# Performance work log

Measured on AMD Instinct MI355X. Metric: run time of the kernel, lower is better.

The kernel has to match this reference:

```python
import jax, jax.numpy as jnp
import numpy as np

DIM = 1024
HEAD_NUM = 8
D_HEAD = DIM // HEAD_NUM
B, S = 4, 2048


def setup_inputs() -> dict:
    key = jax.random.key(0)
    ks = jax.random.split(key, 7)
    scale = 0.02
    return {
        "Q": jax.random.normal(ks[0], (B, S, DIM), dtype=jnp.float32),
        "K": jax.random.normal(ks[1], (B, S, DIM), dtype=jnp.float32),
        "V": jax.random.normal(ks[2], (B, S, DIM), dtype=jnp.float32),
        "W_Q": jax.random.normal(ks[3], (DIM, DIM), dtype=jnp.float32) * scale,
        "W_K": jax.random.normal(ks[4], (DIM, DIM), dtype=jnp.float32) * scale,
        "W_V": jax.random.normal(ks[5], (DIM, DIM), dtype=jnp.float32) * scale,
        "W_O": jax.random.normal(ks[6], (DIM, DIM), dtype=jnp.float32) * scale,
    }


def reference(Q, K, V, W_Q, W_K, W_V, W_O):
    # torch nn.Linear(bias=False): y = x @ W.T
    b, s, d = Q.shape
    h, dh = HEAD_NUM, d // HEAD_NUM

    def proj_split(x, W):
        # split_head: tensor_split along feature dim into h contiguous chunks,
        # stack at dim 1 -> [b, h, s, dh]; equivalent to reshape+transpose.
        y = jnp.einsum('bsd,ed->bse', x, W)
        return y.reshape(b, s, h, dh).transpose(0, 2, 1, 3)

    q = proj_split(Q, W_Q)  # [b,h,s,dh]
    k = proj_split(K, W_K)
    v = proj_split(V, W_V)

    scores = jnp.einsum('bhqd,bhkd->bhqk', q, k) / jnp.sqrt(jnp.float32(dh))
    # FAITHFUL to original: nn.Softmax(dim=1) normalizes over the HEAD axis.
    attn = jax.nn.softmax(scores, axis=1)
    # dropout is identity in eval mode
    ctx = jnp.einsum('bhqk,bhkd->bhqd', attn, v)  # [b,h,s,dh]
    # concat_head: heads concatenated back along feature dim in order
    ctx = ctx.transpose(0, 2, 1, 3).reshape(b, s, d)
    return jnp.einsum('bsd,ed->bse', ctx, W_O)
```

## Files before the change

### kernel.cpp

```cpp
#include <hip/hip_runtime.h>
#include <math.h>
#include <stdint.h>


typedef __attribute__((ext_vector_type(8))) __bf16 bf16x8;
typedef __attribute__((ext_vector_type(4))) __bf16 bf16x4;
typedef __attribute__((ext_vector_type(4))) float  f32x4;

__device__ __forceinline__ f32x4 mfma16(bf16x8 a, bf16x8 b, f32x4 c) {
    return __builtin_amdgcn_mfma_f32_16x16x32_bf16(a, b, c, 0, 0, 0);
}

__device__ __forceinline__ void cp16(void* lds, const void* g) {
    __builtin_amdgcn_global_load_lds(
        (__attribute__((address_space(1))) void*)(void*)(const_cast<void*>(g)),
        (__attribute__((address_space(3))) void*)lds,
        16, 0, 0);
}

__global__ void cast_f32_to_bf16(const float* __restrict__ src,
                                 __bf16* __restrict__ dst, int n4) {
    int i = blockIdx.x * blockDim.x + threadIdx.x;
    const int stride = gridDim.x * blockDim.x;
    for (; i < n4; i += stride) {
        float4 f = ((const float4*)src)[i];
        bf16x4 o;
        o[0] = (__bf16)f.x; o[1] = (__bf16)f.y; o[2] = (__bf16)f.z; o[3] = (__bf16)f.w;
        ((bf16x4*)dst)[i] = o;
    }
}

__global__ void cast4_f32_to_bf16(const float* __restrict__ s0, __bf16* __restrict__ d0,
                                  const float* __restrict__ s1, __bf16* __restrict__ d1,
                                  const float* __restrict__ s2, __bf16* __restrict__ d2,
                                  const float* __restrict__ s3, __bf16* __restrict__ d3,
                                  int n4) {
    const float* s = (blockIdx.y == 0) ? s0 : (blockIdx.y == 1) ? s1
                    : (blockIdx.y == 2) ? s2 : s3;
    __bf16* d = (blockIdx.y == 0) ? d0 : (blockIdx.y == 1) ? d1
               : (blockIdx.y == 2) ? d2 : d3;
    int i = blockIdx.x * blockDim.x + threadIdx.x;
    const int stride = gridDim.x * blockDim.x;
    for (; i < n4; i += stride) {
        float4 f = ((const float4*)s)[i];
        bf16x4 o;
        o[0] = (__bf16)f.x; o[1] = (__bf16)f.y; o[2] = (__bf16)f.z; o[3] = (__bf16)f.w;
        ((bf16x4*)d)[i] = o;
    }
}

template<int MODE>
__global__ __launch_bounds__(256, 2) void gemm_bt(const __bf16* __restrict__ A,
                                                  const __bf16* __restrict__ Bt,
                                                  void* __restrict__ out,
                                                  float scale)
{
    __shared__ __bf16 As[128 * 32];
    __shared__ __bf16 Bs[128 * 32];
    const int tid  = threadIdx.x;
    const int lane = tid & 63;
    const int u = lane >> 4, v = lane & 15;
    const int w = tid >> 6;
    const int wm = (w >> 1) * 64, wn = (w & 1) * 64;
    const long tM = (long)blockIdx.y * 128;
    const int  tN = blockIdx.x * 128;

    f32x4 acc[4][4];
#pragma unroll
    for (int i = 0; i < 4; ++i)
#pragma unroll
        for (int j = 0; j < 4; ++j) acc[i][j] = (f32x4){0.f, 0.f, 0.f, 0.f};

    const int c0 = tid, c1 = tid + 256;
    const int ar0 = c0 >> 2, ak0 = (c0 & 3) * 8;
    const int ar1 = c1 >> 2, ak1 = (c1 & 3) * 8;

    const __bf16* Ab = A  + tM * 1024;
    const __bf16* Bb = Bt + (long)tN * 1024;

    for (int k0 = 0; k0 < 1024; k0 += 32) {
        __syncthreads();
        cp16(&As[ar0 * 32 + ak0], Ab + (long)ar0 * 1024 + k0 + ak0);
        cp16(&As[ar1 * 32 + ak1], Ab + (long)ar1 * 1024 + k0 + ak1);
        cp16(&Bs[ar0 * 32 + ak0], Bb + (long)ar0 * 1024 + k0 + ak0);
        cp16(&Bs[ar1 * 32 + ak1], Bb + (long)ar1 * 1024 + k0 + ak1);
        __syncthreads();

        bf16x8 af[4], bfr[4];
#pragma unroll
        for (int i = 0; i < 4; ++i)
            af[i] = *(const bf16x8*)&As[(wm + i * 16 + v) * 32 + u * 8];
#pragma unroll
        for (int j = 0; j < 4; ++j)
            bfr[j] = *(const bf16x8*)&Bs[(wn + j * 16 + v) * 32 + u * 8];
#pragma unroll
        for (int i = 0; i < 4; ++i)
#pragma unroll
            for (int j = 0; j < 4; ++j)
                acc[i][j] = mfma16(af[i], bfr[j], acc[i][j]);
    }

#pragma unroll
    for (int i = 0; i < 4; ++i) {
#pragma unroll
        for (int j = 0; j < 4; ++j) {
            const long row0 = tM + wm + i * 16 + u * 4;
            const int  col  = tN + wn + j * 16 + v;
            if (MODE == 0) {
                __bf16* o = (__bf16*)out;
#pragma unroll
                for (int r = 0; r < 4; ++r)
                    o[(row0 + r) * 1024 + col] = (__bf16)(acc[i][j][r] * scale);
            } else if (MODE == 1) {
                float* o = (float*)out;
#pragma unroll
                for (int r = 0; r < 4; ++r)
                    o[(row0 + r) * 1024 + col] = acc[i][j][r];
            } else {
                __bf16* o = (__bf16*)out;
                const int bidx = (int)(row0 >> 11);
                const int s    = (int)(row0 & 2047);
                const int h = col >> 7, dh = col & 127;
                bf16x4 pk;
#pragma unroll
                for (int r = 0; r < 4; ++r) pk[r] = (__bf16)acc[i][j][r];
                *(bf16x4*)&o[((long)(bidx * 8 + h) * 128 + dh) * 2048 + s] = pk;
            }
        }
    }
}

__global__ __launch_bounds__(256, 4) void qk_head_softmax(
    const __bf16* __restrict__ kp, const __bf16* __restrict__ qp,
    __bf16* __restrict__ P, int b_base, int q_base)
{
    __shared__ __bf16 As[64 * 32];
    __shared__ __bf16 Bs[128 * 32];
    __shared__ __bf16 tb[128 * 68];
    const int tid  = threadIdx.x;
    const int lane = tid & 63;
    const int u = lane >> 4, v = lane & 15;
    const int w = tid >> 6;
    const int wm = (w >> 1) * 32, wn = (w & 1) * 64;
    const int bloc = blockIdx.z;
    const int b    = b_base + bloc;
    const int k0   = blockIdx.x * 64;
    const int q0l  = blockIdx.y * 128;
    const int q0g  = q_base + q0l;
    const long Cq  = (long)gridDim.y * 128;

    const int ar0 = tid >> 2, ak0 = (tid & 3) * 8;
    const int ar1 = ar0 + 64, ak1 = ak0;

    const __bf16* Ka = kp + ((long)b * 2048 + k0) * 1024;
    const __bf16* Qa = qp + ((long)b * 2048 + q0g) * 1024;

    f32x4 den[2][4];
#pragma unroll
    for (int i = 0; i < 2; ++i)
#pragma unroll
        for (int j = 0; j < 4; ++j) den[i][j] = (f32x4){0.f, 0.f, 0.f, 0.f};

#pragma unroll 1
    for (int h = 0; h < 8; ++h) {
        f32x4 acc[2][4];
#pragma unroll
        for (int i = 0; i < 2; ++i)
#pragma unroll
            for (int j = 0; j < 4; ++j) acc[i][j] = (f32x4){0.f, 0.f, 0.f, 0.f};

#pragma unroll
        for (int kb = 0; kb < 4; ++kb) {
            const int co = h * 128 + kb * 32;
            __syncthreads();
            cp16(&As[ar0 * 32 + ak0], Ka + (long)ar0 * 1024 + co + ak0);
            cp16(&Bs[ar0 * 32 + ak0], Qa + (long)ar0 * 1024 + co + ak0);
            cp16(&Bs[ar1 * 32 + ak1], Qa + (long)ar1 * 1024 + co + ak1);
            __syncthreads();

            bf16x8 af[2], bfr[4];
#pragma unroll
            for (int i = 0; i < 2; ++i)
                af[i] = *(const bf16x8*)&As[(wm + i * 16 + v) * 32 + u * 8];
#pragma unroll
            for (int j = 0; j < 4; ++j)
                bfr[j] = *(const bf16x8*)&Bs[(wn + j * 16 + v) * 32 + u * 8];
#pragma unroll
            for (int i = 0; i < 2; ++i)
#pragma unroll
                for (int j = 0; j < 4; ++j)
                    acc[i][j] = mfma16(af[i], bfr[j], acc[i][j]);
        }
#pragma unroll
        for (int i = 0; i < 2; ++i)
#pragma unroll
            for (int j = 0; j < 4; ++j)
#pragma unroll
                for (int r = 0; r < 4; ++r)
                    den[i][j][r] += __expf(acc[i][j][r]);
    }

#pragma unroll
    for (int i = 0; i < 2; ++i)
#pragma unroll
        for (int j = 0; j < 4; ++j)
#pragma unroll
            for (int r = 0; r < 4; ++r) den[i][j][r] = 1.0f / den[i][j][r];

#pragma unroll 1
    for (int h = 0; h < 8; ++h) {
        f32x4 acc[2][4];
#pragma unroll
        for (int i = 0; i < 2; ++i)
#pragma unroll
            for (int j = 0; j < 4; ++j) acc[i][j] = (f32x4){0.f, 0.f, 0.f, 0.f};

#pragma unroll
        for (int kb = 0; kb < 4; ++kb) {
            const int co = h * 128 + kb * 32;
            __syncthreads();
            cp16(&As[ar0 * 32 + ak0], Ka + (long)ar0 * 1024 + co + ak0);
            cp16(&Bs[ar0 * 32 + ak0], Qa + (long)ar0 * 1024 + co + ak0);
            cp16(&Bs[ar1 * 32 + ak1], Qa + (long)ar1 * 1024 + co + ak1);
            __syncthreads();

            bf16x8 af[2], bfr[4];
#pragma unroll
            for (int i = 0; i < 2; ++i)
                af[i] = *(const bf16x8*)&As[(wm + i * 16 + v) * 32 + u * 8];
#pragma unroll
            for (int j = 0; j < 4; ++j)
                bfr[j] = *(const bf16x8*)&Bs[(wn + j * 16 + v) * 32 + u * 8];
#pragma unroll
            for (int i = 0; i < 2; ++i)
#pragma unroll
                for (int j = 0; j < 4; ++j)
                    acc[i][j] = mfma16(af[i], bfr[j], acc[i][j]);
        }
        __syncthreads();
#pragma unroll
        for (int i = 0; i < 2; ++i)
#pragma unroll
            for (int j = 0; j < 4; ++j) {
                const int kc = wm + i * 16 + u * 4;
                const int qr = wn + j * 16 + v;
                bf16x4 o;
#pragma unroll
                for (int r = 0; r < 4; ++r) {
                    float e = (float)(__bf16)__expf(acc[i][j][r]);
                    o[r] = (__bf16)(e * den[i][j][r]);
                }
                *(bf16x4*)&tb[qr * 68 + kc] = o;
            }
        __syncthreads();
        __bf16* Ph = P + ((long)(bloc * 8 + h) * Cq + q0l) * 2048 + k0;
#pragma unroll
        for (int p = 0; p < 4; ++p) {
            const int qq = p * 32 + (tid >> 3);
            const int kk = (tid & 7) * 8;
            *(bf16x8*)&Ph[(long)qq * 2048 + kk] = *(const bf16x8*)&tb[qq * 68 + kk];
        }
    }
}

__global__ __launch_bounds__(256, 2) void pv_gemm(
    const __bf16* __restrict__ vt, const __bf16* __restrict__ P,
    __bf16* __restrict__ ctx, int b_base, int q_base)
{
    __shared__ __bf16 As[128 * 32];
    __shared__ __bf16 Bs[128 * 32];
    const int tid  = threadIdx.x;
    const int lane = tid & 63;
    const int u = lane >> 4, v = lane & 15;
    const int w = tid >> 6;
    const int wm = (w >> 1) * 64, wn = (w & 1) * 64;
    const int bhl  = blockIdx.y;
    const int bloc = bhl >> 3, h = bhl & 7;
    const int b    = b_base + bloc;
    const int q0l  = blockIdx.x * 128;
    const int q0g  = q_base + q0l;
    const long Cq  = (long)gridDim.x * 128;

    const int c0 = tid, c1 = tid + 256;
    const int ar0 = c0 >> 2, ak0 = (c0 & 3) * 8;
    const int ar1 = c1 >> 2, ak1 = (c1 & 3) * 8;

    const __bf16* Ab = vt + (long)(b * 8 + h) * 128 * 2048;
    const __bf16* Bb = P  + ((long)(bloc * 8 + h) * Cq + q0l) * 2048;

    f32x4 acc[4][4];
#pragma unroll
    for (int i = 0; i < 4; ++i)
#pragma unroll
        for (int j = 0; j < 4; ++j) acc[i][j] = (f32x4){0.f, 0.f, 0.f, 0.f};

    for (int k0 = 0; k0 < 2048; k0 += 32) {
        __syncthreads();
        cp16(&As[ar0 * 32 + ak0], Ab + (long)ar0 * 2048 + k0 + ak0);
        cp16(&As[ar1 * 32 + ak1], Ab + (long)ar1 * 2048 + k0 + ak1);
        cp16(&Bs[ar0 * 32 + ak0], Bb + (long)ar0 * 2048 + k0 + ak0);
        cp16(&Bs[ar1 * 32 + ak1], Bb + (long)ar1 * 2048 + k0 + ak1);
        __syncthreads();

        bf16x8 af[4], bfr[4];
#pragma unroll
        for (int i = 0; i < 4; ++i)
            af[i] = *(const bf16x8*)&As[(wm + i * 16 + v) * 32 + u * 8];
#pragma unroll
        for (int j = 0; j < 4; ++j)
            bfr[j] = *(const bf16x8*)&Bs[(wn + j * 16 + v) * 32 + u * 8];
#pragma unroll
        for (int i = 0; i < 4; ++i)
#pragma unroll
            for (int j = 0; j < 4; ++j)
                acc[i][j] = mfma16(af[i], bfr[j], acc[i][j]);
    }

#pragma unroll
    for (int i = 0; i < 4; ++i) {
#pragma unroll
        for (int j = 0; j < 4; ++j) {
            const int dh0 = wm + i * 16 + u * 4;
            const int q   = q0g + wn + j * 16 + v;
            bf16x4 pk;
#pragma unroll
            for (int r = 0; r < 4; ++r) pk[r] = (__bf16)acc[i][j][r];
            *(bf16x4*)&ctx[((long)b * 2048 + q) * 1024 + h * 128 + dh0] = pk;
        }
    }
}

__global__ __launch_bounds__(256, 2) void attn_softmax_head(
    const __bf16* __restrict__ qp, const __bf16* __restrict__ kp,
    const __bf16* __restrict__ vt, __bf16* __restrict__ ctx)
{
    __shared__ float part[8 * 256];
    __shared__ float pb[4][2][16 * 33];

    const int tid  = threadIdx.x;
    const int lane = tid & 63;
    const int w = tid >> 6;
    const int u = lane >> 4, v = lane & 15;
    const int b  = blockIdx.y;
    const int q0 = blockIdx.x * 16;

    const long qoff = ((long)b * 2048 + q0 + v) * 1024;
    bf16x8 qf[2][4];
#pragma unroll
    for (int hh = 0; hh < 2; ++hh) {
        const int h = 2 * w + hh;
#pragma unroll
        for (int kk = 0; kk < 4; ++kk)
            qf[hh][kk] = *(const bf16x8*)(qp + qoff + h * 128 + kk * 32 + u * 8);
    }

    f32x4 acc[2][8];
#pragma unroll
    for (int hh = 0; hh < 2; ++hh)
#pragma unroll
        for (int dt = 0; dt < 8; ++dt) acc[hh][dt] = (f32x4){0.f, 0.f, 0.f, 0.f};

    for (int kt = 0; kt < 2048; kt += 32) {
        float e[2][2][4];
#pragma unroll
        for (int hh = 0; hh < 2; ++hh) {
            const int h = 2 * w + hh;
#pragma unroll
            for (int t = 0; t < 2; ++t) {
                f32x4 s = (f32x4){0.f, 0.f, 0.f, 0.f};
                const __bf16* kb = kp + ((long)b * 2048 + kt + t * 16 + v) * 1024
                                      + h * 128 + u * 8;
#pragma unroll
                for (int kk = 0; kk < 4; ++kk)
                    s = mfma16(*(const bf16x8*)(kb + kk * 32), qf[hh][kk], s);
#pragma unroll
                for (int r = 0; r < 4; ++r) e[hh][t][r] = __expf(s[r]);
            }
        }
#pragma unroll
        for (int t = 0; t < 2; ++t)
#pragma unroll
            for (int r = 0; r < 4; ++r)
                part[(t * 4 + r) * 256 + w * 64 + lane] = e[0][t][r] + e[1][t][r];
        __syncthreads();
#pragma unroll
        for (int t = 0; t < 2; ++t)
#pragma unroll
            for (int r = 0; r < 4; ++r) {
                const int j = (t * 4 + r) * 256 + lane;
                const float den = part[j] + part[j + 64] + part[j + 128] + part[j + 192];
                const float rinv = 1.0f / den;
                const int kl = t * 16 + u * 4 + r;
                pb[w][0][v * 33 + kl] = e[0][t][r] * rinv;
                pb[w][1][v * 33 + kl] = e[1][t][r] * rinv;
            }
        bf16x8 pf[2];
#pragma unroll
        for (int hh = 0; hh < 2; ++hh)
#pragma unroll
            for (int jj = 0; jj < 8; ++jj)
                pf[hh][jj] = (__bf16)pb[w][hh][v * 33 + u * 8 + jj];
#pragma unroll
        for (int hh = 0; hh < 2; ++hh) {
            const int h = 2 * w + hh;
            const __bf16* vb = vt + ((long)(b * 8 + h) * 128 + v) * 2048 + kt + u * 8;
#pragma unroll
            for (int dt = 0; dt < 8; ++dt)
                acc[hh][dt] = mfma16(*(const bf16x8*)(vb + (long)dt * 16 * 2048),
                                     pf[hh], acc[hh][dt]);
        }
        __syncthreads();
    }

#pragma unroll
    for (int hh = 0; hh < 2; ++hh) {
        const int h = 2 * w + hh;
#pragma unroll
        for (int dt = 0; dt < 8; ++dt) {
            bf16x4 o;
#pragma unroll
            for (int r = 0; r < 4; ++r) o[r] = (__bf16)acc[hh][dt][r];
            *(bf16x4*)(ctx + ((long)b * 2048 + q0 + v) * 1024
                           + h * 128 + dt * 16 + u * 4) = o;
        }
    }
}

extern "C" void kernel_launch(void* const* d_in, const int* in_sizes, int n_in,
                              void* d_out, int out_size, void* d_ws, size_t ws_size,
                              hipStream_t stream)
{
    const float* Q  = (const float*)d_in[0];
    const float* K  = (const float*)d_in[1];
    const float* V  = (const float*)d_in[2];
    const float* WQ = (const float*)d_in[3];
    const float* WK = (const float*)d_in[4];
    const float* WV = (const float*)d_in[5];
    const float* WO = (const float*)d_in[6];

    __bf16* ws = (__bf16*)d_ws;
    __bf16* wq = ws;
    __bf16* wk = wq + 1048576;
    __bf16* wv = wk + 1048576;
    __bf16* wo = wv + 1048576;
    __bf16* xb = wo + 1048576;
    __bf16* qp = xb + 8388608;
    __bf16* kp = qp + 8388608;
    __bf16* vt = kp + 8388608;
    __bf16* pbuf = vt + 8388608;

    const float qscale = 0.08838834764831845f;

    cast4_f32_to_bf16<<<dim3(256, 4), 256, 0, stream>>>(
        WQ, wq, WK, wk, WV, wv, WO, wo, 262144);

    dim3 gg(8, 64), gb(256);
    cast_f32_to_bf16<<<4096, 256, 0, stream>>>(Q, xb, 2097152);
    gemm_bt<0><<<gg, gb, 0, stream>>>(xb, wq, qp, qscale);
    cast_f32_to_bf16<<<4096, 256, 0, stream>>>(K, xb, 2097152);
    gemm_bt<0><<<gg, gb, 0, stream>>>(xb, wk, kp, 1.0f);
    cast_f32_to_bf16<<<4096, 256, 0, stream>>>(V, xb, 2097152);
    gemm_bt<2><<<gg, gb, 0, stream>>>(xb, wv, vt, 1.0f);

    const size_t baseBytes = 37748736ULL * 2ULL;
    const size_t avail = (ws_size > baseBytes) ? ws_size - baseBytes : 0;
    const int cfgs[6][2] = {{4,2048},{2,2048},{1,2048},{1,1024},{1,512},{1,256}};
    int nb = 0, C = 0;
    for (int c = 0; c < 6; ++c) {
        const size_t need = (size_t)cfgs[c][0] * 8 * cfgs[c][1] * 2048 * 2;
        if (need <= avail) { nb = cfgs[c][0]; C = cfgs[c][1]; break; }
    }

    if (nb) {
        for (int bb = 0; bb < 4; bb += nb)
            for (int qq = 0; qq < 2048; qq += C) {
                qk_head_softmax<<<dim3(32, C / 128, nb), gb, 0, stream>>>(
                    kp, qp, pbuf, bb, qq);
                pv_gemm<<<dim3(C / 128, nb * 8), gb, 0, stream>>>(
                    vt, pbuf, xb, bb, qq);
            }
    } else {
        attn_softmax_head<<<dim3(128, 4), gb, 0, stream>>>(qp, kp, vt, xb);
    }

    gemm_bt<1><<<gg, gb, 0, stream>>>(xb, wo, (float*)d_out, 1.0f);
}
```

Before: 502.1 us.

## Batch QKV casts and projections, swizzle QK LDS tiles, shrink PV tiles and chunks

Merges the three input casts into one launch and the three projection GEMMs into a single 3D-grid kernel, using separate bf16 buffers per input so there is no serial reuse of one scratch buffer. The QK-softmax kernel now stages 64-wide K-slices with an XOR-swizzled LDS layout, which removes the padding and halves the barriers per head. The PV GEMM moves to 128x64 tiles for more blocks. The probability chunk configs now cap at 1024 queries, which means more, smaller launches. The workspace footprint grows, which shrinks the space left for the probability buffer.

```diff
diff --git a/kernel.cpp b/kernel.cpp
--- a/kernel.cpp
+++ b/kernel.cpp
@@ -16,18 +16,6 @@
         (__attribute__((address_space(1))) void*)(void*)(const_cast<void*>(g)),
         (__attribute__((address_space(3))) void*)lds,
         16, 0, 0);
-}
-
-__global__ void cast_f32_to_bf16(const float* __restrict__ src,
-                                 __bf16* __restrict__ dst, int n4) {
-    int i = blockIdx.x * blockDim.x + threadIdx.x;
-    const int stride = gridDim.x * blockDim.x;
-    for (; i < n4; i += stride) {
-        float4 f = ((const float4*)src)[i];
-        bf16x4 o;
-        o[0] = (__bf16)f.x; o[1] = (__bf16)f.y; o[2] = (__bf16)f.z; o[3] = (__bf16)f.w;
-        ((bf16x4*)dst)[i] = o;
-    }
 }
 
 __global__ void cast4_f32_to_bf16(const float* __restrict__ s0, __bf16* __restrict__ d0,
@@ -49,6 +37,22 @@
     }
 }
 
+__global__ void cast3_f32_to_bf16(const float* __restrict__ s0, __bf16* __restrict__ d0,
+                                  const float* __restrict__ s1, __bf16* __restrict__ d1,
+                                  const float* __restrict__ s2, __bf16* __restrict__ d2,
+                                  int n4) {
+    const float* s = (blockIdx.y == 0) ? s0 : (blockIdx.y == 1) ? s1 : s2;
+    __bf16* d = (blockIdx.y == 0) ? d0 : (blockIdx.y == 1) ? d1 : d2;
+    int i = blockIdx.x * blockDim.x + threadIdx.x;
+    const int stride = gridDim.x * blockDim.x;
+    for (; i < n4; i += stride) {
+        float4 f = ((const float4*)s)[i];
+        bf16x4 o;
+        o[0] = (__bf16)f.x; o[1] = (__bf16)f.y; o[2] = (__bf16)f.z; o[3] = (__bf16)f.w;
+        ((bf16x4*)d)[i] = o;
+    }
+}
+
 template<int MODE>
 __global__ __launch_bounds__(256, 2) void gemm_bt(const __bf16* __restrict__ A,
                                                   const __bf16* __restrict__ Bt,
@@ -106,25 +110,98 @@
         for (int j = 0; j < 4; ++j) {
             const long row0 = tM + wm + i * 16 + u * 4;
             const int  col  = tN + wn + j * 16 + v;
-            if (MODE == 0) {
-                __bf16* o = (__bf16*)out;
-#pragma unroll
-                for (int r = 0; r < 4; ++r)
-                    o[(row0 + r) * 1024 + col] = (__bf16)(acc[i][j][r] * scale);
-            } else if (MODE == 1) {
+            if (MODE == 1) {
                 float* o = (float*)out;
 #pragma unroll
                 for (int r = 0; r < 4; ++r)
                     o[(row0 + r) * 1024 + col] = acc[i][j][r];
             } else {
                 __bf16* o = (__bf16*)out;
+#pragma unroll
+                for (int r = 0; r < 4; ++r)
+                    o[(row0 + r) * 1024 + col] = (__bf16)(acc[i][j][r] * scale);
+            }
+        }
+    }
+}
+
+__global__ __launch_bounds__(256, 2) void qkv_proj(
+    const __bf16* __restrict__ xq, const __bf16* __restrict__ xk,
+    const __bf16* __restrict__ xv,
+    const __bf16* __restrict__ wq, const __bf16* __restrict__ wk,
+    const __bf16* __restrict__ wv,
+    __bf16* __restrict__ qp, __bf16* __restrict__ kp, __bf16* __restrict__ vtb,
+    float qscale)
+{
+    __shared__ __bf16 As[128 * 32];
+    __shared__ __bf16 Bs[128 * 32];
+    const int z = blockIdx.z;
+    const __bf16* A  = (z == 0) ? xq : (z == 1) ? xk : xv;
+    const __bf16* Bt = (z == 0) ? wq : (z == 1) ? wk : wv;
+    __bf16* out      = (z == 0) ? qp : (z == 1) ? kp : vtb;
+    const float scale = (z == 0) ? qscale : 1.0f;
+
+    const int tid  = threadIdx.x;
+    const int lane = tid & 63;
+    const int u = lane >> 4, v = lane & 15;
+    const int w = tid >> 6;
+    const int wm = (w >> 1) * 64, wn = (w & 1) * 64;
+    const long tM = (long)blockIdx.y * 128;
+    const int  tN = blockIdx.x * 128;
+
+    f32x4 acc[4][4];
+#pragma unroll
+    for (int i = 0; i < 4; ++i)
+#pragma unroll
+        for (int j = 0; j < 4; ++j) acc[i][j] = (f32x4){0.f, 0.f, 0.f, 0.f};
+
+    const int c0 = tid, c1 = tid + 256;
+    const int ar0 = c0 >> 2, ak0 = (c0 & 3) * 8;
+    const int ar1 = c1 >> 2, ak1 = (c1 & 3) * 8;
+
+    const __bf16* Ab = A  + tM * 1024;
+    const __bf16* Bb = Bt + (long)tN * 1024;
+
+    for (int k0 = 0; k0 < 1024; k0 += 32) {
+        __syncthreads();
+        cp16(&As[ar0 * 32 + ak0], Ab + (long)ar0 * 1024 + k0 + ak0);
+        cp16(&As[ar1 * 32 + ak1], Ab + (long)ar1 * 1024 + k0 + ak1);
+        cp16(&Bs[ar0 * 32 + ak0], Bb + (long)ar0 * 1024 + k0 + ak0);
+        cp16(&Bs[ar1 * 32 + ak1], Bb + (long)ar1 * 1024 + k0 + ak1);
+        __syncthreads();
+
+        bf16x8 af[4], bfr[4];
+#pragma unroll
+        for (int i = 0; i < 4; ++i)
+            af[i] = *(const bf16x8*)&As[(wm + i * 16 + v) * 32 + u * 8];
+#pragma unroll
+        for (int j = 0; j < 4; ++j)
+            bfr[j] = *(const bf16x8*)&Bs[(wn + j * 16 + v) * 32 + u * 8];
+#pragma unroll
+        for (int i = 0; i < 4; ++i)
+#pragma unroll
+            for (int j = 0; j < 4; ++j)
+                acc[i][j] = mfma16(af[i], bfr[j], acc[i][j]);
+    }
+
+#pragma unroll
+    for (int i = 0; i < 4; ++i) {
+#pragma unroll
+        for (int j = 0; j < 4; ++j) {
+            const long row0 = tM + wm + i * 16 + u * 4;
+            const int  col  = tN + wn + j * 16 + v;
+            if (z < 2) {
+#pragma unroll
+                for (int r = 0; r < 4; ++r)
+                    out[(row0 + r) * 1024 + col] = (__bf16)(acc[i][j][r] * scale);
+            } else {
                 const int bidx = (int)(row0 >> 11);
                 const int s    = (int)(row0 & 2047);
                 const int h = col >> 7, dh = col & 127;
                 bf16x4 pk;
 #pragma unroll
                 for (int r = 0; r < 4; ++r) pk[r] = (__bf16)acc[i][j][r];
-                *(bf16x4*)&o[((long)(bidx * 8 + h) * 128 + dh) * 2048 + s] = pk;
+                *(bf16x4*)&out[((long)(bidx * 8 + h) * 128 + dh) * 2048 + s] = pk;
             }
         }
     }
@@ -134,9 +211,9 @@
     const __bf16* __restrict__ kp, const __bf16* __restrict__ qp,
     __bf16* __restrict__ P, int b_base, int q_base)
 {
-    __shared__ __bf16 As[64 * 32];
-    __shared__ __bf16 Bs[128 * 32];
-    __shared__ __bf16 tb[128 * 68];
+    __shared__ __bf16 As[64 * 64];
+    __shared__ __bf16 Bs[128 * 64];
+    __shared__ __bf16 tb[128 * 64];
     const int tid  = threadIdx.x;
     const int lane = tid & 63;
     const int u = lane >> 4, v = lane & 15;
@@ -149,8 +226,8 @@
     const int q0g  = q_base + q0l;
     const long Cq  = (long)gridDim.y * 128;
 
-    const int ar0 = tid >> 2, ak0 = (tid & 3) * 8;
-    const int ar1 = ar0 + 64, ak1 = ak0;
+    const int sr = tid >> 3;
+    const int sc = tid & 7;
 
     const __bf16* Ka = kp + ((long)b * 2048 + k0) * 1024;
     const __bf16* Qa = qp + ((long)b * 2048 + q0g) * 1024;
@@ -170,26 +247,44 @@
             for (int j = 0; j < 4; ++j) acc[i][j] = (f32x4){0.f, 0.f, 0.f, 0.f};
 
 #pragma unroll
-        for (int kb = 0; kb < 4; ++kb) {
-            const int co = h * 128 + kb * 32;
+        for (int kb = 0; kb < 2; ++kb) {
+            const int co = h * 128 + kb * 64;
             __syncthreads();
-            cp16(&As[ar0 * 32 + ak0], Ka + (long)ar0 * 1024 + co + ak0);
-            cp16(&Bs[ar0 * 32 + ak0], Qa + (long)ar0 * 1024 + co + ak0);
-            cp16(&Bs[ar1 * 32 + ak1], Qa + (long)ar1 * 1024 + co + ak1);
+#pragma unroll
+            for (int t = 0; t < 2; ++t) {
+                const int r = sr + 32 * t;
+                cp16(&As[r * 64 + sc * 8],
+                     Ka + (long)r * 1024 + co + (sc ^ (r & 7)) * 8);
+            }
+#pragma unroll
+            for (int t = 0; t < 4; ++t) {
+                const int r = sr + 32 * t;
+                cp16(&Bs[r * 64 + sc * 8],
+                     Qa + (long)r * 1024 + co + (sc ^ (r & 7)) * 8);
+            }
             __syncthreads();
 
-            bf16x8 af[2], bfr[4];
-#pragma unroll
-            for (int i = 0; i < 2; ++i)
-                af[i] = *(const bf16x8*)&As[(wm + i * 16 + v) * 32 + u * 8];
-#pragma unroll
-            for (int j = 0; j < 4; ++j)
-                bfr[j] = *(const bf16x8*)&Bs[(wn + j * 16 + v) * 32 + u * 8];
-#pragma unroll
-            for (int i = 0; i < 2; ++i)
-#pragma unroll
-                for (int j = 0; j < 4; ++j)
-                    acc[i][j] = mfma16(af[i], bfr[j], acc[i][j]);
+#pragma unroll
+            for (int ks = 0; ks < 2; ++ks) {
+                bf16x8 af[2], bfr[4];
+#pragma unroll
+                for (int i = 0; i < 2; ++i) {
+                    const int r = wm + i * 16 + v;
+                    af[i] = *(const bf16x8*)&As[r * 64 +
+                               ((ks * 32 + u * 8) ^ ((v & 7) * 8))];
+                }
+#pragma unroll
+                for (int j = 0; j < 4; ++j) {
+                    const int r = wn + j * 16 + v;
+                    bfr[j] = *(const bf16x8*)&Bs[r * 64 +
+                               ((ks * 32 + u * 8) ^ ((v & 7) * 8))];
+                }
+#pragma unroll
+                for (int i = 0; i < 2; ++i)
+#pragma unroll
+                    for (int j = 0; j < 4; ++j)
+                        acc[i][j] = mfma16(af[i], bfr[j], acc[i][j]);
+            }
         }
 #pragma unroll
         for (int i = 0; i < 2; ++i)
@@ -216,26 +311,44 @@
             for (int j = 0; j < 4; ++j) acc[i][j] = (f32x4){0.f, 0.f, 0.f, 0.f};
 
 #pragma unroll
-        for (int kb = 0; kb < 4; ++kb) {
-            const int co = h * 128 + kb * 32;
+        for (int kb = 0; kb < 2; ++kb) {
+            const int co = h * 128 + kb * 64;
             __syncthreads();
-            cp16(&As[ar0 * 32 + ak0], Ka + (long)ar0 * 1024 + co + ak0);
-            cp16(&Bs[ar0 * 32 + ak0], Qa + (long)ar0 * 1024 + co + ak0);
-            cp16(&Bs[ar1 * 32 + ak1], Qa + (long)ar1 * 1024 + co + ak1);
+#pragma unroll
+            for (int t = 0; t < 2; ++t) {
+                const int r = sr + 32 * t;
+                cp16(&As[r * 64 + sc * 8],
+                     Ka + (long)r * 1024 + co + (sc ^ (r & 7)) * 8);
+            }
+#pragma unroll
+            for (int t = 0; t < 4; ++t) {
+                const int r = sr + 32 * t;
+                cp16(&Bs[r * 64 + sc * 8],
+                     Qa + (long)r * 1024 + co + (sc ^ (r & 7)) * 8);
+            }
             __syncthreads();
 
-            bf16x8 af[2], bfr[4];
-#pragma unroll
-            for (int i = 0; i < 2; ++i)
-                af[i] = *(const bf16x8*)&As[(wm + i * 16 + v) * 32 + u * 8];
-#pragma unroll
-            for (int j = 0; j < 4; ++j)
-                bfr[j] = *(const bf16x8*)&Bs[(wn + j * 16 + v) * 32 + u * 8];
-#pragma unroll
-            for (int i = 0; i < 2; ++i)
-#pragma unroll
-                for (int j = 0; j < 4; ++j)
-                    acc[i][j] = mfma16(af[i], bfr[j], acc[i][j]);
+#pragma unroll
+            for (int ks = 0; ks < 2; ++ks) {
+                bf16x8 af[2], bfr[4];
+#pragma unroll
+                for (int i = 0; i < 2; ++i) {
+                    const int r = wm + i * 16 + v;
+                    af[i] = *(const bf16x8*)&As[r * 64 +
+                               ((ks * 32 + u * 8) ^ ((v & 7) * 8))];
+                }
+#pragma unroll
+                for (int j = 0; j < 4; ++j) {
+                    const int r = wn + j * 16 + v;
+                    bfr[j] = *(const bf16x8*)&Bs[r * 64 +
+                               ((ks * 32 + u * 8) ^ ((v & 7) * 8))];
+                }
+#pragma unroll
+                for (int i = 0; i < 2; ++i)
+#pragma unroll
+                    for (int j = 0; j < 4; ++j)
+                        acc[i][j] = mfma16(af[i], bfr[j], acc[i][j]);
+            }
         }
         __syncthreads();
 #pragma unroll
@@ -250,7 +363,7 @@
                     float e = (float)(__bf16)__expf(acc[i][j][r]);
                     o[r] = (__bf16)(e * den[i][j][r]);
                 }
-                *(bf16x4*)&tb[qr * 68 + kc] = o;
+                *(bf16x4*)&tb[qr * 64 + (kc ^ ((qr & 7) * 8))] = o;
             }
         __syncthreads();
         __bf16* Ph = P + ((long)(bloc * 8 + h) * Cq + q0l) * 2048 + k0;
@@ -258,7 +371,8 @@
         for (int p = 0; p < 4; ++p) {
             const int qq = p * 32 + (tid >> 3);
             const int kk = (tid & 7) * 8;
-            *(bf16x8*)&Ph[(long)qq * 2048 + kk] = *(const bf16x8*)&tb[qq * 68 + kk];
+            *(bf16x8*)&Ph[(long)qq * 2048 + kk] =
+                *(const bf16x8*)&tb[qq * 64 + (kk ^ ((qq & 7) * 8))];
         }
     }
 }
@@ -268,58 +382,55 @@
     __bf16* __restrict__ ctx, int b_base, int q_base)
 {
     __shared__ __bf16 As[128 * 32];
-    __shared__ __bf16 Bs[128 * 32];
+    __shared__ __bf16 Bs[64 * 32];
     const int tid  = threadIdx.x;
     const int lane = tid & 63;
     const int u = lane >> 4, v = lane & 15;
     const int w = tid >> 6;
-    const int wm = (w >> 1) * 64, wn = (w & 1) * 64;
+    const int wm = (w >> 1) * 64, wn = (w & 1) * 32;
     const int bhl  = blockIdx.y;
     const int bloc = bhl >> 3, h = bhl & 7;
     const int b    = b_base + bloc;
-    const int q0l  = blockIdx.x * 128;
+    const int q0l  = blockIdx.x * 64;
     const int q0g  = q_base + q0l;
-    const long Cq  = (long)gridDim.x * 128;
-
-    const int c0 = tid, c1 = tid + 256;
-    const int ar0 = c0 >> 2, ak0 = (c0 & 3) * 8;
-    const int ar1 = c1 >> 2, ak1 = (c1 & 3) * 8;
+    const long Cq  = (long)gridDim.x * 64;
+
+    const int ar0 = tid >> 2, ak = (tid & 3) * 8;
 
     const __bf16* Ab = vt + (long)(b * 8 + h) * 128 * 2048;
     const __bf16* Bb = P  + ((long)(bloc * 8 + h) * Cq + q0l) * 2048;
 
-    f32x4 acc[4][4];
+    f32x4 acc[4][2];
 #pragma unroll
     for (int i = 0; i < 4; ++i)
 #pragma unroll
-        for (int j = 0; j < 4; ++j) acc[i][j] = (f32x4){0.f, 0.f, 0.f, 0.f};
+        for (int j = 0; j < 2; ++j) acc[i][j] = (f32x4){0.f, 0.f, 0.f, 0.f};
 
     for (int k0 = 0; k0 < 2048; k0 += 32) {
         __syncthreads();
-        cp16(&As[ar0 * 32 + ak0], Ab + (long)ar0 * 2048 + k0 + ak0);
-        cp16(&As[ar1 * 32 + ak1], Ab + (long)ar1 * 2048 + k0 + ak1);
-        cp16(&Bs[ar0 * 32 + ak0], Bb + (long)ar0 * 2048 + k0 + ak0);
-        cp16(&Bs[ar1 * 32 + ak1], Bb + (long)ar1 * 2048 + k0 + ak1);
-        __syncthreads();
-
-        bf16x8 af[4], bfr[4];
+        cp16(&As[ar0 * 32 + ak], Ab + (long)ar0 * 2048 + k0 + ak);
+        cp16(&As[(ar0 + 64) * 32 + ak], Ab + (long)(ar0 + 64) * 2048 + k0 + ak);
+        cp16(&Bs[ar0 * 32 + ak], Bb + (long)ar0 * 2048 + k0 + ak);
+        __syncthreads();
+
+        bf16x8 af[4], bfr[2];
 #pragma unroll
         for (int i = 0; i < 4; ++i)
             af[i] = *(const bf16x8*)&As[(wm + i * 16 + v) * 32 + u * 8];
 #pragma unroll
-        for (int j = 0; j < 4; ++j)
+        for (int j = 0; j < 2; ++j)
             bfr[j] = *(const bf16x8*)&Bs[(wn + j * 16 + v) * 32 + u * 8];
 #pragma unroll
         for (int i = 0; i < 4; ++i)
 #pragma unroll
-            for (int j = 0; j < 4; ++j)
+            for (int j = 0; j < 2; ++j)
                 acc[i][j] = mfma16(af[i], bfr[j], acc[i][j]);
     }
 
 #pragma unroll
     for (int i = 0; i < 4; ++i) {
 #pragma unroll
-        for (int j = 0; j < 4; ++j) {
+        for (int j = 0; j < 2; ++j) {
             const int dh0 = wm + i * 16 + u * 4;
             const int q   = q0g + wn + j * 16 + v;
             bf16x4 pk;
@@ -443,30 +554,29 @@
     __bf16* wk = wq + 1048576;
     __bf16* wv = wk + 1048576;
     __bf16* wo = wv + 1048576;
-    __bf16* xb = wo + 1048576;
-    __bf16* qp = xb + 8388608;
+    __bf16* xq = wo + 1048576;
+    __bf16* xk = xq + 8388608;
+    __bf16* xv = xk + 8388608;
+    __bf16* qp = xv + 8388608;
     __bf16* kp = qp + 8388608;
     __bf16* vt = kp + 8388608;
-    __bf16* pbuf = vt + 8388608;
+    __bf16* xb = vt + 8388608;
+    __bf16* pbuf = xb + 8388608;
 
     const float qscale = 0.08838834764831845f;
 
     cast4_f32_to_bf16<<<dim3(256, 4), 256, 0, stream>>>(
         WQ, wq, WK, wk, WV, wv, WO, wo, 262144);
-
-    dim3 gg(8, 64), gb(256);
-    cast_f32_to_bf16<<<4096, 256, 0, stream>>>(Q, xb, 2097152);
-    gemm_bt<0><<<gg, gb, 0, stream>>>(xb, wq, qp, qscale);
-    cast_f32_to_bf16<<<4096, 256, 0, stream>>>(K, xb, 2097152);
-    gemm_bt<0><<<gg, gb, 0, stream>>>(xb, wk, kp, 1.0f);
-    cast_f32_to_bf16<<<4096, 256, 0, stream>>>(V, xb, 2097152);
-    gemm_bt<2><<<gg, gb, 0, stream>>>(xb, wv, vt, 1.0f);
-
-    const size_t baseBytes = 37748736ULL * 2ULL;
+    cast3_f32_to_bf16<<<dim3(2048, 3), 256, 0, stream>>>(
+        Q, xq, K, xk, V, xv, 2097152);
+    qkv_proj<<<dim3(8, 64, 3), 256, 0, stream>>>(
+        xq, xk, xv, wq, wk, wv, qp, kp, vt, qscale);
+
+    const size_t baseBytes = 62914560ULL * 2ULL;
     const size_t avail = (ws_size > baseBytes) ? ws_size - baseBytes : 0;
-    const int cfgs[6][2] = {{4,2048},{2,2048},{1,2048},{1,1024},{1,512},{1,256}};
+    const int cfgs[5][2] = {{4,1024},{4,512},{2,512},{1,512},{1,256}};
     int nb = 0, C = 0;
-    for (int c = 0; c < 6; ++c) {
+    for (int c = 0; c < 5; ++c) {
         const size_t need = (size_t)cfgs[c][0] * 8 * cfgs[c][1] * 2048 * 2;
         if (need <= avail) { nb = cfgs[c][0]; C = cfgs[c][1]; break; }
     }
@@ -474,14 +584,14 @@
     if (nb) {
         for (int bb = 0; bb < 4; bb += nb)
             for (int qq = 0; qq < 2048; qq += C) {
-                qk_head_softmax<<<dim3(32, C / 128, nb), gb, 0, stream>>>(
+                qk_head_softmax<<<dim3(32, C / 128, nb), 256, 0, stream>>>(
                     kp, qp, pbuf, bb, qq);
-                pv_gemm<<<dim3(C / 128, nb * 8), gb, 0, stream>>>(
+                pv_gemm<<<dim3(C / 64, nb * 8), 256, 0, stream>>>(
                     vt, pbuf, xb, bb, qq);
             }
     } else {
-        attn_softmax_head<<<dim3(128, 4), gb, 0, stream>>>(qp, kp, vt, xb);
-    }
-
-    gemm_bt<1><<<gg, gb, 0, stream>>>(xb, wo, (float*)d_out, 1.0f);
-}
+        attn_softmax_head<<<dim3(128, 4), 256, 0, stream>>>(qp, kp, vt, xb);
+    }
+
+    gemm_bt<1><<<dim3(8, 64), 256, 0, stream>>>(xb, wo, (float*)d_out, 1.0f);
+}
```

After: 486.1 us. 1.03x faster.
